# Performance work log

Measured on AMD Instinct MI355X. Metric: run time of the kernel, lower is better.

The kernel has to match this reference:

```python
import jax, jax.numpy as jnp
import numpy as np

ATTN_LEN = 128  # init_kwargs attn_len


def _lstm(x, Wih, Whh, bih, bhh):
    """PyTorch-style LSTM (gate order i,f,g,o), scanning over axis 0 of x.
    x: (S, N, H_in) -> (S, N, H). Matches nn.LSTM applied to the given layout."""
    H = Whh.shape[1]
    n = x.shape[1]
    xp = x @ Wih.T + bih + bhh  # precompute input projection, fold both biases

    def step(carry, xt):
        h, c = carry
        gates = xt + h @ Whh.T
        i, f, g, o = jnp.split(gates, 4, axis=-1)
        i = jax.nn.sigmoid(i)
        f = jax.nn.sigmoid(f)
        g = jnp.tanh(g)
        o = jax.nn.sigmoid(o)
        c = f * c + i * g
        h = o * jnp.tanh(c)
        return (h, c), h

    init = (jnp.zeros((n, H), x.dtype), jnp.zeros((n, H), x.dtype))
    _, hs = jax.lax.scan(step, init, xp)
    return hs


def setup_inputs() -> dict:
    key = jax.random.key(0)
    ks = jax.random.split(key, 16)
    F_in, H = 257, 256
    B, T = 8, 2048
    s = 1.0 / np.sqrt(H)

    def w(k, shape):
        return jax.random.uniform(k, shape, jnp.float32, -s, s)

    return {
        "x": jax.random.normal(ks[0], (B, T, F_in), jnp.float32),
        "feat_w": w(ks[1], (H, F_in)), "feat_b": w(ks[2], (H,)),
        "k_Wih": w(ks[3], (4 * H, H)), "k_Whh": w(ks[4], (4 * H, H)),
        "k_bih": w(ks[5], (4 * H,)), "k_bhh": w(ks[6], (4 * H,)),
        "q_Wih": w(ks[7], (4 * H, H)), "q_Whh": w(ks[8], (4 * H, H)),
        "q_bih": w(ks[9], (4 * H,)), "q_bhh": w(ks[10], (4 * H,)),
        "score_w": w(ks[11], (H, H)),
        "enhance_w": w(ks[12], (H, 2 * H)), "enhance_b": w(ks[13], (H,)),
        "mask_w": w(ks[14], (F_in, H)), "mask_b": w(ks[15], (F_in,)),
    }


def reference(x, feat_w, feat_b, k_Wih, k_Whh, k_bih, k_bhh,
              q_Wih, q_Whh, q_bih, q_bhh, score_w,
              enhance_w, enhance_b, mask_w, mask_b):
    input_x = x
    h = jnp.tanh(x @ feat_w.T + feat_b)          # (B,T,H); dropout_p=0 -> identity
    # Faithful to source: nn.LSTM without batch_first scans along dim0 of x.
    k = _lstm(h, k_Wih, k_Whh, k_bih, k_bhh)     # (B,T,H)
    q = _lstm(h, q_Wih, q_Whh, q_bih, q_bhh)     # stacked_encoder=False -> q_enc(x)

    # bmm(score(q), k^T): batched over dim0, attention over dims 1-2
    s = jnp.einsum('bth,bsh->bts', q @ score_w.T, k)
    e = jnp.exp(s - jnp.max(s, axis=-1, keepdims=True))
    T = s.shape[-1]
    band = jnp.tril(jnp.ones((T, T), x.dtype)) * jnp.triu(jnp.ones((T, T), x.dtype), -ATTN_LEN)
    w_ = e * band                                 # tril then triu(-attn_len)
    w_ = w_ / (jnp.sum(w_, axis=-1, keepdims=True) + 1e-10)
    c = jnp.einsum('bts,bsh->bth', w_, k)

    out = jnp.tanh(jnp.concatenate([c, q], axis=-1) @ enhance_w.T + enhance_b)
    m = jax.nn.sigmoid(out @ mask_w.T + mask_b)
    return input_x * m, w_
```

## Files before the change

kernel.cpp:

```cpp
#include <hip/hip_runtime.h>
#include <math.h>


#define Bq 8
#define Tq 2048
#define Fq 257
#define Hq 256
#define Gq 1024
#define TH (Tq*Hq)
#define KW 192
#define PLD 40
#define KTLD 40
#define Mq (Bq*Tq)

typedef __bf16 bf16_t;
typedef __bf16 bf16x8 __attribute__((ext_vector_type(8)));
typedef float f32x4 __attribute__((ext_vector_type(4)));

__device__ __forceinline__ float sigf(float x) { return 1.0f / (1.0f + __expf(-x)); }
__device__ __forceinline__ float tanh_f(float x) { return 1.0f - 2.0f / (__expf(2.0f * x) + 1.0f); }

#define CV_X   (Mq*288)
#define CV_FW  (256*288)
#define CV_WIH (2048*256)
#define CV_WHH (2048*256)
#define CV_SC  (256*256)
#define CV_EN  (256*512)
#define CV_MK  (384*256)
#define CV_O1  CV_X
#define CV_O2  (CV_O1+CV_FW)
#define CV_O3  (CV_O2+CV_WIH)
#define CV_O4  (CV_O3+CV_WHH)
#define CV_O5  (CV_O4+CV_SC)
#define CV_O6  (CV_O5+CV_EN)
#define CV_TOT (CV_O6+CV_MK)

__global__ __launch_bounds__(256) void cvt_all(
    const float* __restrict__ x, const float* __restrict__ feat_w,
    const float* __restrict__ kWih, const float* __restrict__ kWhh,
    const float* __restrict__ qWih, const float* __restrict__ qWhh,
    const float* __restrict__ scorew, const float* __restrict__ enhw,
    const float* __restrict__ maskw, bf16_t* __restrict__ dst)
{
    const int base = (blockIdx.x * 256 + threadIdx.x) * 8;
    if (base >= CV_TOT) return;
    bf16_t v[8];
#pragma unroll
    for (int e = 0; e < 8; ++e) {
        const int i = base + e;
        float f;
        if (i < CV_O1)      { const int r = i / 288, c = i - r * 288;
                              f = (c < Fq) ? x[(size_t)r * Fq + c] : 0.0f; }
        else if (i < CV_O2) { const int i2 = i - CV_O1, r = i2 / 288, c = i2 - r * 288;
                              f = (c < Fq) ? feat_w[r * Fq + c] : 0.0f; }
        else if (i < CV_O3) { const int i2 = i - CV_O2, r = i2 >> 8, c = i2 & 255;
                              f = (r < 1024) ? kWih[r * 256 + c] : qWih[(r - 1024) * 256 + c]; }
        else if (i < CV_O4) { const int i2 = i - CV_O3, r = i2 >> 8, c = i2 & 255;
                              f = (r < 1024) ? kWhh[r * 256 + c] : qWhh[(r - 1024) * 256 + c]; }
        else if (i < CV_O5) { f = scorew[i - CV_O4]; }
        else if (i < CV_O6) { f = enhw[i - CV_O5]; }
        else                { const int i2 = i - CV_O6, r = i2 >> 8, c = i2 & 255;
                              f = (r < Fq) ? maskw[r * 256 + c] : 0.0f; }
        v[e] = (bf16_t)f;
    }
    *(bf16x8*)(dst + base) = *(bf16x8*)v;
}

__global__ void bias_fold(const float* __restrict__ kbih, const float* __restrict__ kbhh,
                          const float* __restrict__ qbih, const float* __restrict__ qbhh,
                          float* __restrict__ out)
{
    const int i = blockIdx.x * 256 + threadIdx.x;
    out[i] = (i < 1024) ? kbih[i] + kbhh[i] : qbih[i - 1024] + qbhh[i - 1024];
}

__device__ __forceinline__ const bf16_t* seg_ptr(
    const bf16_t* __restrict__ A1, int lda1, int K1,
    const bf16_t* __restrict__ A2, int lda2, int row, int k, int col8)
{
    return (k < K1) ? A1 + (size_t)row * lda1 + k + col8
                    : A2 + (size_t)row * lda2 + (k - K1) + col8;
}

template<int ACT, bool MULX, bool BF16OUT, bool F32OUT>
__global__ __launch_bounds__(256) void gemm_mfma(
    const bf16_t* __restrict__ A1, int lda1, int K1,
    const bf16_t* __restrict__ A2, int lda2, int K2,
    const bf16_t* __restrict__ W,
    const float* __restrict__ bias,
    const float* __restrict__ xm, int ldx,
    float* __restrict__ out, bf16_t* __restrict__ outbf, int ldo, int Nlog)
{
    __shared__ __align__(16) bf16_t As[64 * 32];
    __shared__ __align__(16) bf16_t Ws[128 * 32];
    const int tid = threadIdx.x;
    const int lane = tid & 63;
    const int wave = tid >> 6;
    const int wr = wave >> 1, wc = wave & 1;
    const int fr = lane & 15;
    const int fo = (lane >> 4) * 8;
    const int srow = tid >> 2;
    const int scol = (tid & 3) * 8;
    const int m0 = blockIdx.y * 64, n0 = blockIdx.x * 128;

    const int K = K1 + K2;
    const int ldw = K;

    uint4 ar = *(const uint4*)seg_ptr(A1, lda1, K1, A2, lda2, m0 + srow, 0, scol);
    uint4 w0 = *(const uint4*)(W + (size_t)(n0 + srow)      * ldw + scol);
    uint4 w1 = *(const uint4*)(W + (size_t)(n0 + srow + 64) * ldw + scol);

    f32x4 acc[2][4] = {};
    for (int k0 = 0; k0 < K; k0 += 32) {
        __syncthreads();
        *(uint4*)&As[srow * 32 + scol]        = ar;
        *(uint4*)&Ws[srow * 32 + scol]        = w0;
        *(uint4*)&Ws[(srow + 64) * 32 + scol] = w1;
        if (k0 + 32 < K) {
            ar = *(const uint4*)seg_ptr(A1, lda1, K1, A2, lda2, m0 + srow, k0 + 32, scol);
            w0 = *(const uint4*)(W + (size_t)(n0 + srow)      * ldw + k0 + 32 + scol);
            w1 = *(const uint4*)(W + (size_t)(n0 + srow + 64) * ldw + k0 + 32 + scol);
        }
        __syncthreads();
        bf16x8 af[2], bfr[4];
#pragma unroll
        for (int i = 0; i < 2; ++i) af[i]  = *(const bf16x8*)&As[(wr * 32 + i * 16 + fr) * 32 + fo];
#pragma unroll
        for (int j = 0; j < 4; ++j) bfr[j] = *(const bf16x8*)&Ws[(wc * 64 + j * 16 + fr) * 32 + fo];
#pragma unroll
        for (int i = 0; i < 2; ++i)
#pragma unroll
            for (int j = 0; j < 4; ++j)
                acc[i][j] = __builtin_amdgcn_mfma_f32_16x16x32_bf16(af[i], bfr[j], acc[i][j], 0, 0, 0);
    }

    const int rbase = (lane >> 4) * 4;
#pragma unroll
    for (int i = 0; i < 2; ++i) {
#pragma unroll
        for (int j = 0; j < 4; ++j) {
            const int n = n0 + wc * 64 + j * 16 + fr;
            if (n >= Nlog) continue;
            const float bv = bias ? bias[n] : 0.0f;
            const int m = m0 + wr * 32 + i * 16 + rbase;
#pragma unroll
            for (int r = 0; r < 4; ++r) {
                float v = acc[i][j][r] + bv;
                if (ACT == 1) v = tanh_f(v);
                else if (ACT == 2) v = sigf(v);
                if (MULX) v *= xm[(size_t)(m + r) * ldx + n];
                if (F32OUT) out[(size_t)(m + r) * ldo + n] = v;
                if (BF16OUT) outbf[(size_t)(m + r) * ldo + n] = (bf16_t)v;
            }
        }
    }
}

__global__ __launch_bounds__(256) void lstm_step(
    const bf16_t* __restrict__ hkp, const bf16_t* __restrict__ hqp,
    const bf16_t* __restrict__ Whh_all,
    const float* __restrict__ xp_b,
    float* __restrict__ ck, float* __restrict__ cq,
    bf16_t* __restrict__ hk, bf16_t* __restrict__ hq)
{
    __shared__ __align__(16) bf16_t As[64 * 32];
    __shared__ __align__(16) bf16_t Ws[128 * 32];
    const int z = blockIdx.z;
    const bf16_t* hprev = z ? hqp : hkp;
    const bf16_t* Wbase = Whh_all + (size_t)z * 1024 * 256;
    float* c     = z ? cq : ck;
    bf16_t* hout = z ? hq : hk;

    const int tid = threadIdx.x, lane = tid & 63, wave = tid >> 6;
    const int wr = wave >> 1, wc = wave & 1;
    const int fr = lane & 15, rg = lane >> 4, fo = rg * 8;
    const int m0 = blockIdx.y * 64;
    const int jb = blockIdx.x * 32;

    f32x4 acc[2][4] = {};

    if (hprev) {
        const int arow = tid >> 2, acol = (tid & 3) * 8;
        const int s0 = tid >> 2, s1 = s0 + 64;
        const int wn0 = ((s0 >> 5) * 256) + jb + (s0 & 31);
        const int wn1 = ((s1 >> 5) * 256) + jb + (s1 & 31);
        uint4 ar  = *(const uint4*)(hprev + (size_t)(m0 + arow) * Hq + acol);
        uint4 w0r = *(const uint4*)(Wbase + (size_t)wn0 * 256 + acol);
        uint4 w1r = *(const uint4*)(Wbase + (size_t)wn1 * 256 + acol);
#pragma unroll
        for (int t = 0; t < 8; ++t) {
            if (t) __syncthreads();
            *(uint4*)&As[arow * 32 + acol] = ar;
            *(uint4*)&Ws[s0 * 32 + acol]   = w0r;
            *(uint4*)&Ws[s1 * 32 + acol]   = w1r;
            if (t < 7) {
                const int k = (t + 1) * 32;
                ar  = *(const uint4*)(hprev + (size_t)(m0 + arow) * Hq + k + acol);
                w0r = *(const uint4*)(Wbase + (size_t)wn0 * 256 + k + acol);
                w1r = *(const uint4*)(Wbase + (size_t)wn1 * 256 + k + acol);
            }
            __syncthreads();
            bf16x8 af[2], bg[4];
#pragma unroll
            for (int i = 0; i < 2; ++i) af[i] = *(const bf16x8*)&As[(wr * 32 + i * 16 + fr) * 32 + fo];
#pragma unroll
            for (int g = 0; g < 4; ++g) bg[g] = *(const bf16x8*)&Ws[(g * 32 + wc * 16 + fr) * 32 + fo];
#pragma unroll
            for (int i = 0; i < 2; ++i)
#pragma unroll
                for (int g = 0; g < 4; ++g)
                    acc[i][g] = __builtin_amdgcn_mfma_f32_16x16x32_bf16(af[i], bg[g], acc[i][g], 0, 0, 0);
        }
    }

    const int j = jb + wc * 16 + fr;
#pragma unroll
    for (int i = 0; i < 2; ++i) {
#pragma unroll
        for (int r = 0; r < 4; ++r) {
            const int t = m0 + wr * 32 + i * 16 + rg * 4 + r;
            const float* xpr = xp_b + (size_t)t * 2048 + (size_t)z * 1024;
            const float gi = acc[i][0][r] + xpr[j];
            const float gf = acc[i][1][r] + xpr[256 + j];
            const float gg = acc[i][2][r] + xpr[512 + j];
            const float go = acc[i][3][r] + xpr[768 + j];
            const size_t ix = (size_t)t * Hq + j;
            const float cn = sigf(gf) * c[ix] + sigf(gi) * tanh_f(gg);
            c[ix] = cn;
            hout[ix] = (bf16_t)(sigf(go) * tanh_f(cn));
        }
    }
}

__global__ __launch_bounds__(256) void band_fused(
    const bf16_t* __restrict__ qsbf, const bf16_t* __restrict__ kbf,
    float* __restrict__ out1, bf16_t* __restrict__ c_att)
{
    __shared__ __align__(16) bf16_t Ks[8 * KW * 32];
    __shared__ __align__(16) bf16_t P[6 * 64 * PLD];
    __shared__ __align__(16) bf16_t KT[256 * KTLD];

    const int b = blockIdx.y;
    const int t0 = blockIdx.x * 64;
    const int u0 = t0 - 128;
    const int tid = threadIdx.x, lane = tid & 63, w = tid >> 6;
    const int fr = lane & 15, rg = lane >> 4, fo = rg * 8;
    const size_t kbase = (size_t)b * Tq;

#pragma unroll
    for (int it = 0; it < 24; ++it) {
        const int idx = it * 256 + tid;
        const int n  = idx >> 5;
        const int c8 = (idx & 31) * 8;
        uint4 v = {0, 0, 0, 0};
        const int u = u0 + n;
        if (u >= 0) v = *(const uint4*)(kbf + (kbase + u) * (size_t)Hq + c8);
        *(uint4*)&Ks[((c8 >> 5) * KW + n) * 32 + (c8 & 31)] = v;
    }
    __syncthreads();

    f32x4 acc[12] = {};
    const bf16_t* qrow = qsbf + (kbase + t0 + 16 * w + fr) * (size_t)Hq;
#pragma unroll
    for (int ks = 0; ks < 8; ++ks) {
        const bf16x8 aq = *(const bf16x8*)(qrow + ks * 32 + fo);
#pragma unroll
        for (int jf = 0; jf < 12; ++jf) {
            const bf16x8 bk = *(const bf16x8*)&Ks[(ks * KW + jf * 16 + fr) * 32 + fo];
            acc[jf] = __builtin_amdgcn_mfma_f32_16x16x32_bf16(aq, bk, acc[jf], 0, 0, 0);
        }
    }

    const int jmin = (128 - t0) > 0 ? (128 - t0) : 0;
    float mx[4] = {-3e38f, -3e38f, -3e38f, -3e38f};
#pragma unroll
    for (int jf = 0; jf < 12; ++jf)
#pragma unroll
        for (int r = 0; r < 4; ++r) {
            const int i = 16 * w + rg * 4 + r;
            const int j = jf * 16 + fr;
            if (j >= i && j <= i + 128 && j >= jmin)
                mx[r] = fmaxf(mx[r], acc[jf][r]);
        }
#pragma unroll
    for (int d = 1; d < 16; d <<= 1)
#pragma unroll
        for (int r = 0; r < 4; ++r) mx[r] = fmaxf(mx[r], __shfl_xor(mx[r], d));

    float ex[12][4];
    float sm[4] = {0.0f, 0.0f, 0.0f, 0.0f};
#pragma unroll
    for (int jf = 0; jf < 12; ++jf)
#pragma unroll
        for (int r = 0; r < 4; ++r) {
            const int i = 16 * w + rg * 4 + r;
            const int j = jf * 16 + fr;
            const bool v = (j >= i && j <= i + 128 && j >= jmin);
            const float e = v ? __expf(acc[jf][r] - mx[r]) : 0.0f;
            ex[jf][r] = e;
            sm[r] += e;
        }
#pragma unroll
    for (int d = 1; d < 16; d <<= 1)
#pragma unroll
        for (int r = 0; r < 4; ++r) sm[r] += __shfl_xor(sm[r], d);
    float inv[4];
#pragma unroll
    for (int r = 0; r < 4; ++r) inv[r] = 1.0f / (sm[r] + 1e-10f);

#pragma unroll
    for (int jf = 0; jf < 12; ++jf)
#pragma unroll
        for (int r = 0; r < 4; ++r) {
            const int i = 16 * w + rg * 4 + r;
            const int j = jf * 16 + fr;
            const float wv = ex[jf][r] * inv[r];
            if (u0 + j >= 0)
                out1[(kbase + t0 + i) * (size_t)Tq + (u0 + j)] = wv;
            P[((j >> 5) * 64 + i) * PLD + (j & 31)] = (bf16_t)wv;
        }

    {
        const int c4l = (u0 > 0 ? u0 : 0) >> 2;
        const int c4r = (u0 + KW) >> 2;
        const float4 z4 = {0.0f, 0.0f, 0.0f, 0.0f};
        for (int rr = 0; rr < 16; ++rr) {
            float* rowp = out1 + (kbase + t0 + 16 * w + rr) * (size_t)Tq;
            for (int c4 = lane; c4 < c4l; c4 += 64)
                *(float4*)(rowp + 4 * c4) = z4;
            for (int c4 = c4r + lane; c4 < Tq / 4; c4 += 64)
                *(float4*)(rowp + 4 * c4) = z4;
        }
    }

    f32x4 cacc[16] = {};
    for (int jc = 0; jc < 6; ++jc) {
        __syncthreads();
#pragma unroll
        for (int it = 0; it < 4; ++it) {
            const int idx = it * 256 + tid;
            const int jl = idx >> 5;
            const int hc = (idx & 31) * 8;
            const bf16x8 kv = *(const bf16x8*)&Ks[((hc >> 5) * KW + jc * 32 + jl) * 32 + (hc & 31)];
#pragma unroll
            for (int e = 0; e < 8; ++e) KT[(hc + e) * KTLD + jl] = kv[e];
        }
        __syncthreads();
        const bf16x8 pa = *(const bf16x8*)&P[(jc * 64 + 16 * w + fr) * PLD + fo];
#pragma unroll
        for (int hf = 0; hf < 16; ++hf) {
            const bf16x8 bk = *(const bf16x8*)&KT[(hf * 16 + fr) * KTLD + fo];
            cacc[hf] = __builtin_amdgcn_mfma_f32_16x16x32_bf16(pa, bk, cacc[hf], 0, 0, 0);
        }
    }

#pragma unroll
    for (int hf = 0; hf < 16; ++hf)
#pragma unroll
        for (int r = 0; r < 4; ++r) {
            const int i = 16 * w + rg * 4 + r;
            c_att[(kbase + t0 + i) * (size_t)Hq + hf * 16 + fr] = (bf16_t)cacc[hf][r];
        }
}

extern "C" void kernel_launch(void* const* d_in, const int* in_sizes, int n_in,
                              void* d_out, int out_size, void* d_ws, size_t ws_size,
                              hipStream_t stream)
{
    (void)in_sizes; (void)n_in; (void)out_size; (void)ws_size;
    const float* x        = (const float*)d_in[0];
    const float* feat_w   = (const float*)d_in[1];
    const float* feat_b   = (const float*)d_in[2];
    const float* k_Wih    = (const float*)d_in[3];
    const float* k_Whh    = (const float*)d_in[4];
    const float* k_bih    = (const float*)d_in[5];
    const float* k_bhh    = (const float*)d_in[6];
    const float* q_Wih    = (const float*)d_in[7];
    const float* q_Whh    = (const float*)d_in[8];
    const float* q_bih    = (const float*)d_in[9];
    const float* q_bhh    = (const float*)d_in[10];
    const float* score_w  = (const float*)d_in[11];
    const float* enhance_w= (const float*)d_in[12];
    const float* enhance_b= (const float*)d_in[13];
    const float* mask_w   = (const float*)d_in[14];
    const float* mask_b   = (const float*)d_in[15];

    float* out0 = (float*)d_out;
    float* out1 = out0 + (size_t)Bq * Tq * Fq;

    float* cst      = (float*)d_ws;
    float* bias_all = cst + (size_t)2 * TH;
    float* xp       = bias_all + 2048;
    bf16_t* cvd = (bf16_t*)(xp + (size_t)Mq * 2048);
    bf16_t* xbf     = cvd;
    bf16_t* featw   = cvd + CV_O1;
    bf16_t* Wih_all = cvd + CV_O2;
    bf16_t* Whh_all = cvd + CV_O3;
    bf16_t* scw     = cvd + CV_O4;
    bf16_t* enw     = cvd + CV_O5;
    bf16_t* mkw     = cvd + CV_O6;
    bf16_t* hfeatbf = cvd + CV_TOT;
    bf16_t* hkbf    = hfeatbf + (size_t)Mq * Hq;
    bf16_t* hqbf    = hkbf + (size_t)Bq * TH;
    bf16_t* cattb   = hqbf + (size_t)Bq * TH;

    float* ck = cst;
    float* cq = cst + TH;

    hipMemsetAsync(cst, 0, (size_t)2 * TH * sizeof(float), stream);

    cvt_all<<<CV_TOT / 8 / 256, 256, 0, stream>>>(
        x, feat_w, k_Wih, k_Whh, q_Wih, q_Whh, score_w, enhance_w, mask_w, cvd);
    bias_fold<<<8, 256, 0, stream>>>(k_bih, k_bhh, q_bih, q_bhh, bias_all);

    gemm_mfma<1, false, true, false><<<dim3(2, Mq / 64), 256, 0, stream>>>(
        xbf, 288, 288, nullptr, 0, 0, featw, feat_b, nullptr, 0,
        nullptr, hfeatbf, Hq, 1 << 30);

    gemm_mfma<0, false, false, true><<<dim3(16, Mq / 64), 256, 0, stream>>>(
        hfeatbf, Hq, Hq, nullptr, 0, 0, Wih_all, bias_all, nullptr, 0,
        xp, nullptr, 2048, 2048);

    for (int b = 0; b < Bq; ++b) {
        const bf16_t* pk = b ? hkbf + (size_t)(b - 1) * TH : nullptr;
        const bf16_t* pq = b ? hqbf + (size_t)(b - 1) * TH : nullptr;
        lstm_step<<<dim3(8, Tq / 64, 2), 256, 0, stream>>>(
            pk, pq, Whh_all, xp + (size_t)b * Tq * 2048, ck, cq,
            hkbf + (size_t)b * TH, hqbf + (size_t)b * TH);
    }

    bf16_t* qsbf = xbf;
    gemm_mfma<0, false, true, false><<<dim3(2, Mq / 64), 256, 0, stream>>>(
        hqbf, Hq, Hq, nullptr, 0, 0, scw, nullptr, nullptr, 0,
        nullptr, qsbf, Hq, 1 << 30);

    band_fused<<<dim3(Tq / 64, Bq), 256, 0, stream>>>(qsbf, hkbf, out1, cattb);

    bf16_t* outh = hfeatbf;
    gemm_mfma<1, false, true, false><<<dim3(2, Mq / 64), 256, 0, stream>>>(
        cattb, Hq, Hq, hqbf, Hq, Hq, enw, enhance_b, nullptr, 0,
        nullptr, outh, Hq, 1 << 30);

    gemm_mfma<2, true, false, true><<<dim3(3, Mq / 64), 256, 0, stream>>>(
        outh, Hq, Hq, nullptr, 0, 0, mkw, mask_b, x, Fq,
        out0, nullptr, Fq, Fq);
}
```

Measured before the change: 254.1 us.

## Fuse LSTM input projection into recurrent step kernel with concatenated weights

Drops the separate input-projection GEMM and its large fp32 xp buffer. Each LSTM step kernel now runs a K=512 GEMM over [h_feat, h_prev] against concatenated [Wih|Whh] bf16 weights and adds the folded bias in the epilogue. The first step is a template specialization that skips the previous-hidden part and the c read, which removes the memset. Bias folding also moves into the conversion kernel, so two launches go away. The recurrent chain does more GEMM work per step, but the step kernels no longer write and re-read the 128MB fp32 intermediate.

```diff
diff --git a/kernel.cpp b/kernel.cpp
--- a/kernel.cpp
+++ b/kernel.cpp
@@ -6,7 +6,6 @@
 #define Tq 2048
 #define Fq 257
 #define Hq 256
-#define Gq 1024
 #define TH (Tq*Hq)
 #define KW 192
 #define PLD 40
@@ -22,28 +21,41 @@
 
 #define CV_X   (Mq*288)
 #define CV_FW  (256*288)
-#define CV_WIH (2048*256)
-#define CV_WHH (2048*256)
+#define CV_WK  (1024*512)
+#define CV_WQ  (1024*512)
 #define CV_SC  (256*256)
 #define CV_EN  (256*512)
 #define CV_MK  (384*256)
 #define CV_O1  CV_X
 #define CV_O2  (CV_O1+CV_FW)
-#define CV_O3  (CV_O2+CV_WIH)
-#define CV_O4  (CV_O3+CV_WHH)
+#define CV_O3  (CV_O2+CV_WK)
+#define CV_O4  (CV_O3+CV_WQ)
 #define CV_O5  (CV_O4+CV_SC)
 #define CV_O6  (CV_O5+CV_EN)
 #define CV_TOT (CV_O6+CV_MK)
+#define CVB    (CV_TOT/8/256)
 
 __global__ __launch_bounds__(256) void cvt_all(
     const float* __restrict__ x, const float* __restrict__ feat_w,
     const float* __restrict__ kWih, const float* __restrict__ kWhh,
     const float* __restrict__ qWih, const float* __restrict__ qWhh,
     const float* __restrict__ scorew, const float* __restrict__ enhw,
-    const float* __restrict__ maskw, bf16_t* __restrict__ dst)
-{
+    const float* __restrict__ maskw, bf16_t* __restrict__ dst,
+    const float* __restrict__ kbih, const float* __restrict__ kbhh,
+    const float* __restrict__ qbih, const float* __restrict__ qbhh,
+    float* __restrict__ bias_all)
+{
+    if (blockIdx.x == CVB) {
+        const int i0 = threadIdx.x * 8;
+#pragma unroll
+        for (int e = 0; e < 8; ++e) {
+            const int i = i0 + e;
+            bias_all[i] = (i < 1024) ? kbih[i] + kbhh[i]
+                                     : qbih[i - 1024] + qbhh[i - 1024];
+        }
+        return;
+    }
     const int base = (blockIdx.x * 256 + threadIdx.x) * 8;
-    if (base >= CV_TOT) return;
     bf16_t v[8];
 #pragma unroll
     for (int e = 0; e < 8; ++e) {
@@ -53,10 +65,10 @@
                               f = (c < Fq) ? x[(size_t)r * Fq + c] : 0.0f; }
         else if (i < CV_O2) { const int i2 = i - CV_O1, r = i2 / 288, c = i2 - r * 288;
                               f = (c < Fq) ? feat_w[r * Fq + c] : 0.0f; }
-        else if (i < CV_O3) { const int i2 = i - CV_O2, r = i2 >> 8, c = i2 & 255;
-                              f = (r < 1024) ? kWih[r * 256 + c] : qWih[(r - 1024) * 256 + c]; }
-        else if (i < CV_O4) { const int i2 = i - CV_O3, r = i2 >> 8, c = i2 & 255;
-                              f = (r < 1024) ? kWhh[r * 256 + c] : qWhh[(r - 1024) * 256 + c]; }
+        else if (i < CV_O3) { const int i2 = i - CV_O2, r = i2 >> 9, c = i2 & 511;
+                              f = (c < 256) ? kWih[r * 256 + c] : kWhh[r * 256 + c - 256]; }
+        else if (i < CV_O4) { const int i2 = i - CV_O3, r = i2 >> 9, c = i2 & 511;
+                              f = (c < 256) ? qWih[r * 256 + c] : qWhh[r * 256 + c - 256]; }
         else if (i < CV_O5) { f = scorew[i - CV_O4]; }
         else if (i < CV_O6) { f = enhw[i - CV_O5]; }
         else                { const int i2 = i - CV_O6, r = i2 >> 8, c = i2 & 255;
@@ -64,14 +76,6 @@
         v[e] = (bf16_t)f;
     }
     *(bf16x8*)(dst + base) = *(bf16x8*)v;
-}
-
-__global__ void bias_fold(const float* __restrict__ kbih, const float* __restrict__ kbhh,
-                          const float* __restrict__ qbih, const float* __restrict__ qbhh,
-                          float* __restrict__ out)
-{
-    const int i = blockIdx.x * 256 + threadIdx.x;
-    out[i] = (i < 1024) ? kbih[i] + kbhh[i] : qbih[i - 1024] + qbhh[i - 1024];
 }
 
 __device__ __forceinline__ const bf16_t* seg_ptr(
@@ -156,19 +160,20 @@
     }
 }
 
+template<bool FIRST>
 __global__ __launch_bounds__(256) void lstm_step(
+    const bf16_t* __restrict__ hfb,
     const bf16_t* __restrict__ hkp, const bf16_t* __restrict__ hqp,
-    const bf16_t* __restrict__ Whh_all,
-    const float* __restrict__ xp_b,
-    float* __restrict__ ck, float* __restrict__ cq,
+    const bf16_t* __restrict__ Wall, const float* __restrict__ bias_all,
+    float* __restrict__ cst,
     bf16_t* __restrict__ hk, bf16_t* __restrict__ hq)
 {
     __shared__ __align__(16) bf16_t As[64 * 32];
     __shared__ __align__(16) bf16_t Ws[128 * 32];
     const int z = blockIdx.z;
     const bf16_t* hprev = z ? hqp : hkp;
-    const bf16_t* Wbase = Whh_all + (size_t)z * 1024 * 256;
-    float* c     = z ? cq : ck;
+    const bf16_t* Wz = Wall + (size_t)z * (1024 * 512);
+    float* c     = cst + (size_t)z * TH;
     bf16_t* hout = z ? hq : hk;
 
     const int tid = threadIdx.x, lane = tid & 63, wave = tid >> 6;
@@ -177,59 +182,64 @@
     const int m0 = blockIdx.y * 64;
     const int jb = blockIdx.x * 32;
 
+    const int s0 = tid >> 2, acol = (tid & 3) * 8;
+    const int s1 = s0 + 64;
+    const int wn0 = ((s0 >> 5) * 256) + jb + (s0 & 31);
+    const int wn1 = ((s1 >> 5) * 256) + jb + (s1 & 31);
+
+    constexpr int NIT = FIRST ? 8 : 16;
+
     f32x4 acc[2][4] = {};
 
-    if (hprev) {
-        const int arow = tid >> 2, acol = (tid & 3) * 8;
-        const int s0 = tid >> 2, s1 = s0 + 64;
-        const int wn0 = ((s0 >> 5) * 256) + jb + (s0 & 31);
-        const int wn1 = ((s1 >> 5) * 256) + jb + (s1 & 31);
-        uint4 ar  = *(const uint4*)(hprev + (size_t)(m0 + arow) * Hq + acol);
-        uint4 w0r = *(const uint4*)(Wbase + (size_t)wn0 * 256 + acol);
-        uint4 w1r = *(const uint4*)(Wbase + (size_t)wn1 * 256 + acol);
-#pragma unroll
-        for (int t = 0; t < 8; ++t) {
-            if (t) __syncthreads();
-            *(uint4*)&As[arow * 32 + acol] = ar;
-            *(uint4*)&Ws[s0 * 32 + acol]   = w0r;
-            *(uint4*)&Ws[s1 * 32 + acol]   = w1r;
-            if (t < 7) {
-                const int k = (t + 1) * 32;
-                ar  = *(const uint4*)(hprev + (size_t)(m0 + arow) * Hq + k + acol);
-                w0r = *(const uint4*)(Wbase + (size_t)wn0 * 256 + k + acol);
-                w1r = *(const uint4*)(Wbase + (size_t)wn1 * 256 + k + acol);
-            }
-            __syncthreads();
-            bf16x8 af[2], bg[4];
-#pragma unroll
-            for (int i = 0; i < 2; ++i) af[i] = *(const bf16x8*)&As[(wr * 32 + i * 16 + fr) * 32 + fo];
-#pragma unroll
-            for (int g = 0; g < 4; ++g) bg[g] = *(const bf16x8*)&Ws[(g * 32 + wc * 16 + fr) * 32 + fo];
-#pragma unroll
-            for (int i = 0; i < 2; ++i)
-#pragma unroll
-                for (int g = 0; g < 4; ++g)
-                    acc[i][g] = __builtin_amdgcn_mfma_f32_16x16x32_bf16(af[i], bg[g], acc[i][g], 0, 0, 0);
-        }
+    uint4 ar  = *(const uint4*)(hfb + (size_t)(m0 + s0) * Hq + acol);
+    uint4 w0r = *(const uint4*)(Wz + (size_t)wn0 * 512 + acol);
+    uint4 w1r = *(const uint4*)(Wz + (size_t)wn1 * 512 + acol);
+#pragma unroll
+    for (int t = 0; t < NIT; ++t) {
+        if (t) __syncthreads();
+        *(uint4*)&As[s0 * 32 + acol] = ar;
+        *(uint4*)&Ws[s0 * 32 + acol] = w0r;
+        *(uint4*)&Ws[s1 * 32 + acol] = w1r;
+        if (t + 1 < NIT) {
+            const int tn = t + 1;
+            ar  = (tn < 8)
+                ? *(const uint4*)(hfb   + (size_t)(m0 + s0) * Hq + tn * 32 + acol)
+                : *(const uint4*)(hprev + (size_t)(m0 + s0) * Hq + (tn - 8) * 32 + acol);
+            w0r = *(const uint4*)(Wz + (size_t)wn0 * 512 + tn * 32 + acol);
+            w1r = *(const uint4*)(Wz + (size_t)wn1 * 512 + tn * 32 + acol);
+        }
+        __syncthreads();
+        bf16x8 af[2], bg[4];
+#pragma unroll
+        for (int i = 0; i < 2; ++i) af[i] = *(const bf16x8*)&As[(wr * 32 + i * 16 + fr) * 32 + fo];
+#pragma unroll
+        for (int g = 0; g < 4; ++g) bg[g] = *(const bf16x8*)&Ws[(g * 32 + wc * 16 + fr) * 32 + fo];
+#pragma unroll
+        for (int i = 0; i < 2; ++i)
+#pragma unroll
+            for (int g = 0; g < 4; ++g)
+                acc[i][g] = __builtin_amdgcn_mfma_f32_16x16x32_bf16(af[i], bg[g], acc[i][g], 0, 0, 0);
     }
 
     const int j = jb + wc * 16 + fr;
-#pragma unroll
-    for (int i = 0; i < 2; ++i) {
+    float bs[4];
+#pragma unroll
+    for (int g = 0; g < 4; ++g) bs[g] = bias_all[z * 1024 + g * 256 + j];
+#pragma unroll
+    for (int i = 0; i < 2; ++i)
 #pragma unroll
         for (int r = 0; r < 4; ++r) {
             const int t = m0 + wr * 32 + i * 16 + rg * 4 + r;
-            const float* xpr = xp_b + (size_t)t * 2048 + (size_t)z * 1024;
-            const float gi = acc[i][0][r] + xpr[j];
-            const float gf = acc[i][1][r] + xpr[256 + j];
-            const float gg = acc[i][2][r] + xpr[512 + j];
-            const float go = acc[i][3][r] + xpr[768 + j];
             const size_t ix = (size_t)t * Hq + j;
-            const float cn = sigf(gf) * c[ix] + sigf(gi) * tanh_f(gg);
+            const float gi = acc[i][0][r] + bs[0];
+            const float gf = acc[i][1][r] + bs[1];
+            const float gg = acc[i][2][r] + bs[2];
+            const float go = acc[i][3][r] + bs[3];
+            const float cn = FIRST ? sigf(gi) * tanh_f(gg)
+                                   : sigf(gf) * c[ix] + sigf(gi) * tanh_f(gg);
             c[ix] = cn;
             hout[ix] = (bf16_t)(sigf(go) * tanh_f(cn));
         }
-    }
 }
 
 __global__ __launch_bounds__(256) void band_fused(
@@ -390,12 +400,10 @@
 
     float* cst      = (float*)d_ws;
     float* bias_all = cst + (size_t)2 * TH;
-    float* xp       = bias_all + 2048;
-    bf16_t* cvd = (bf16_t*)(xp + (size_t)Mq * 2048);
+    bf16_t* cvd = (bf16_t*)(bias_all + 2048);
     bf16_t* xbf     = cvd;
     bf16_t* featw   = cvd + CV_O1;
-    bf16_t* Wih_all = cvd + CV_O2;
-    bf16_t* Whh_all = cvd + CV_O3;
+    bf16_t* Wall    = cvd + CV_O2;
     bf16_t* scw     = cvd + CV_O4;
     bf16_t* enw     = cvd + CV_O5;
     bf16_t* mkw     = cvd + CV_O6;
@@ -404,30 +412,22 @@
     bf16_t* hqbf    = hkbf + (size_t)Bq * TH;
     bf16_t* cattb   = hqbf + (size_t)Bq * TH;
 
-    float* ck = cst;
-    float* cq = cst + TH;
-
-    hipMemsetAsync(cst, 0, (size_t)2 * TH * sizeof(float), stream);
-
-    cvt_all<<<CV_TOT / 8 / 256, 256, 0, stream>>>(
-        x, feat_w, k_Wih, k_Whh, q_Wih, q_Whh, score_w, enhance_w, mask_w, cvd);
-    bias_fold<<<8, 256, 0, stream>>>(k_bih, k_bhh, q_bih, q_bhh, bias_all);
+    cvt_all<<<CVB + 1, 256, 0, stream>>>(
+        x, feat_w, k_Wih, k_Whh, q_Wih, q_Whh, score_w, enhance_w, mask_w, cvd,
+        k_bih, k_bhh, q_bih, q_bhh, bias_all);
 
     gemm_mfma<1, false, true, false><<<dim3(2, Mq / 64), 256, 0, stream>>>(
         xbf, 288, 288, nullptr, 0, 0, featw, feat_b, nullptr, 0,
         nullptr, hfeatbf, Hq, 1 << 30);
 
-    gemm_mfma<0, false, false, true><<<dim3(16, Mq / 64), 256, 0, stream>>>(
-        hfeatbf, Hq, Hq, nullptr, 0, 0, Wih_all, bias_all, nullptr, 0,
-        xp, nullptr, 2048, 2048);
-
-    for (int b = 0; b < Bq; ++b) {
-        const bf16_t* pk = b ? hkbf + (size_t)(b - 1) * TH : nullptr;
-        const bf16_t* pq = b ? hqbf + (size_t)(b - 1) * TH : nullptr;
-        lstm_step<<<dim3(8, Tq / 64, 2), 256, 0, stream>>>(
-            pk, pq, Whh_all, xp + (size_t)b * Tq * 2048, ck, cq,
+    lstm_step<true><<<dim3(8, Tq / 64, 2), 256, 0, stream>>>(
+        hfeatbf, nullptr, nullptr, Wall, bias_all, cst, hkbf, hqbf);
+    for (int b = 1; b < Bq; ++b)
+        lstm_step<false><<<dim3(8, Tq / 64, 2), 256, 0, stream>>>(
+            hfeatbf + (size_t)b * TH,
+            hkbf + (size_t)(b - 1) * TH, hqbf + (size_t)(b - 1) * TH,
+            Wall, bias_all, cst,
             hkbf + (size_t)b * TH, hqbf + (size_t)b * TH);
-    }
 
     bf16_t* qsbf = xbf;
     gemm_mfma<0, false, true, false><<<dim3(2, Mq / 64), 256, 0, stream>>>(
```

Measured after the change: 209.9 us. 17.4% less time.

## Fuse first LSTM step into input-projection GEMM and merge bias fold into conversion

Applied to the files above, without the earlier changes.

Replaces the generic input-projection GEMM with a gate-interleaved xp_gemm kernel. For the first batch slice (zero initial state) it applies the LSTM cell directly and writes c and h, so there is no xp write for that slice, no memset of the cell state, and no first lstm_step launch. The bias folding moves into an extra block of the conversion kernel, which saves one launch. The costs are a specialised kernel layout and dropping the forget-gate term, which relies on the initial state being zero.

```diff
diff --git a/kernel.cpp b/kernel.cpp
--- a/kernel.cpp
+++ b/kernel.cpp
@@ -6,7 +6,6 @@
 #define Tq 2048
 #define Fq 257
 #define Hq 256
-#define Gq 1024
 #define TH (Tq*Hq)
 #define KW 192
 #define PLD 40
@@ -34,16 +33,29 @@
 #define CV_O5  (CV_O4+CV_SC)
 #define CV_O6  (CV_O5+CV_EN)
 #define CV_TOT (CV_O6+CV_MK)
+#define CVB    (CV_TOT/8/256)
 
 __global__ __launch_bounds__(256) void cvt_all(
     const float* __restrict__ x, const float* __restrict__ feat_w,
     const float* __restrict__ kWih, const float* __restrict__ kWhh,
     const float* __restrict__ qWih, const float* __restrict__ qWhh,
     const float* __restrict__ scorew, const float* __restrict__ enhw,
-    const float* __restrict__ maskw, bf16_t* __restrict__ dst)
-{
+    const float* __restrict__ maskw, bf16_t* __restrict__ dst,
+    const float* __restrict__ kbih, const float* __restrict__ kbhh,
+    const float* __restrict__ qbih, const float* __restrict__ qbhh,
+    float* __restrict__ bias_all)
+{
+    if (blockIdx.x == CVB) {
+        const int i0 = threadIdx.x * 8;
+#pragma unroll
+        for (int e = 0; e < 8; ++e) {
+            const int i = i0 + e;
+            bias_all[i] = (i < 1024) ? kbih[i] + kbhh[i]
+                                     : qbih[i - 1024] + qbhh[i - 1024];
+        }
+        return;
+    }
     const int base = (blockIdx.x * 256 + threadIdx.x) * 8;
-    if (base >= CV_TOT) return;
     bf16_t v[8];
 #pragma unroll
     for (int e = 0; e < 8; ++e) {
@@ -66,14 +78,6 @@
     *(bf16x8*)(dst + base) = *(bf16x8*)v;
 }
 
-__global__ void bias_fold(const float* __restrict__ kbih, const float* __restrict__ kbhh,
-                          const float* __restrict__ qbih, const float* __restrict__ qbhh,
-                          float* __restrict__ out)
-{
-    const int i = blockIdx.x * 256 + threadIdx.x;
-    out[i] = (i < 1024) ? kbih[i] + kbhh[i] : qbih[i - 1024] + qbhh[i - 1024];
-}
-
 __device__ __forceinline__ const bf16_t* seg_ptr(
     const bf16_t* __restrict__ A1, int lda1, int K1,
     const bf16_t* __restrict__ A2, int lda2, int row, int k, int col8)
@@ -156,6 +160,95 @@
     }
 }
 
+__global__ __launch_bounds__(256) void xp_gemm(
+    const bf16_t* __restrict__ hfeat,
+    const bf16_t* __restrict__ Wih_all,
+    const float* __restrict__ bias_all,
+    float* __restrict__ xp,
+    float* __restrict__ cst,
+    bf16_t* __restrict__ hk0, bf16_t* __restrict__ hq0)
+{
+    __shared__ __align__(16) bf16_t As[64 * 32];
+    __shared__ __align__(16) bf16_t Ws[128 * 32];
+    const int z = blockIdx.z;
+    const bf16_t* Wz = Wih_all + (size_t)z * (1024 * 256);
+
+    const int tid = threadIdx.x, lane = tid & 63, wave = tid >> 6;
+    const int wr = wave >> 1, wc = wave & 1;
+    const int fr = lane & 15, rg = lane >> 4, fo = rg * 8;
+    const int m0 = blockIdx.y * 64;
+    const int jb = blockIdx.x * 32;
+
+    const int s0 = tid >> 2, acol = (tid & 3) * 8;
+    const int s1 = s0 + 64;
+    const int wn0 = ((s0 >> 5) * 256) + jb + (s0 & 31);
+    const int wn1 = ((s1 >> 5) * 256) + jb + (s1 & 31);
+
+    f32x4 acc[2][4] = {};
+    uint4 ar  = *(const uint4*)(hfeat + (size_t)(m0 + s0) * Hq + acol);
+    uint4 w0r = *(const uint4*)(Wz + (size_t)wn0 * 256 + acol);
+    uint4 w1r = *(const uint4*)(Wz + (size_t)wn1 * 256 + acol);
+#pragma unroll
+    for (int t = 0; t < 8; ++t) {
+        if (t) __syncthreads();
+        *(uint4*)&As[s0 * 32 + acol] = ar;
+        *(uint4*)&Ws[s0 * 32 + acol] = w0r;
+        *(uint4*)&Ws[s1 * 32 + acol] = w1r;
+        if (t < 7) {
+            const int k = (t + 1) * 32;
+            ar  = *(const uint4*)(hfeat + (size_t)(m0 + s0) * Hq + k + acol);
+            w0r = *(const uint4*)(Wz + (size_t)wn0 * 256 + k + acol);
+            w1r = *(const uint4*)(Wz + (size_t)wn1 * 256 + k + acol);
+        }
+        __syncthreads();
+        bf16x8 af[2], bg[4];
+#pragma unroll
+        for (int i = 0; i < 2; ++i) af[i] = *(const bf16x8*)&As[(wr * 32 + i * 16 + fr) * 32 + fo];
+#pragma unroll
+        for (int g = 0; g < 4; ++g) bg[g] = *(const bf16x8*)&Ws[(g * 32 + wc * 16 + fr) * 32 + fo];
+#pragma unroll
+        for (int i = 0; i < 2; ++i)
+#pragma unroll
+            for (int g = 0; g < 4; ++g)
+                acc[i][g] = __builtin_amdgcn_mfma_f32_16x16x32_bf16(af[i], bg[g], acc[i][g], 0, 0, 0);
+    }
+
+    const int j = jb + wc * 16 + fr;
+    float bs[4];
+#pragma unroll
+    for (int g = 0; g < 4; ++g) bs[g] = bias_all[z * 1024 + g * 256 + j];
+
+    if (m0 < Tq) {
+        float* c = cst + (size_t)z * TH;
+        bf16_t* hout = z ? hq0 : hk0;
+#pragma unroll
+        for (int i = 0; i < 2; ++i)
+#pragma unroll
+            for (int r = 0; r < 4; ++r) {
+                const int t = m0 + wr * 32 + i * 16 + rg * 4 + r;
+                const size_t ix = (size_t)t * Hq + j;
+                const float gi = acc[i][0][r] + bs[0];
+                const float gg = acc[i][2][r] + bs[2];
+                const float go = acc[i][3][r] + bs[3];
+                const float cn = sigf(gi) * tanh_f(gg);
+                c[ix] = cn;
+                hout[ix] = (bf16_t)(sigf(go) * tanh_f(cn));
+            }
+    } else {
+#pragma unroll
+        for (int i = 0; i < 2; ++i)
+#pragma unroll
+            for (int r = 0; r < 4; ++r) {
+                const int t = m0 + wr * 32 + i * 16 + rg * 4 + r;
+                float* xpr = xp + (size_t)t * 2048 + (size_t)z * 1024;
+                xpr[j]       = acc[i][0][r] + bs[0];
+                xpr[256 + j] = acc[i][1][r] + bs[1];
+                xpr[512 + j] = acc[i][2][r] + bs[2];
+                xpr[768 + j] = acc[i][3][r] + bs[3];
+            }
+    }
+}
+
 __global__ __launch_bounds__(256) void lstm_step(
     const bf16_t* __restrict__ hkp, const bf16_t* __restrict__ hqp,
     const bf16_t* __restrict__ Whh_all,
@@ -179,7 +272,7 @@
 
     f32x4 acc[2][4] = {};
 
-    if (hprev) {
+    {
         const int arow = tid >> 2, acol = (tid & 3) * 8;
         const int s0 = tid >> 2, s1 = s0 + 64;
         const int wn0 = ((s0 >> 5) * 256) + jb + (s0 & 31);
@@ -407,27 +500,22 @@
     float* ck = cst;
     float* cq = cst + TH;
 
-    hipMemsetAsync(cst, 0, (size_t)2 * TH * sizeof(float), stream);
-
-    cvt_all<<<CV_TOT / 8 / 256, 256, 0, stream>>>(
-        x, feat_w, k_Wih, k_Whh, q_Wih, q_Whh, score_w, enhance_w, mask_w, cvd);
-    bias_fold<<<8, 256, 0, stream>>>(k_bih, k_bhh, q_bih, q_bhh, bias_all);
+    cvt_all<<<CVB + 1, 256, 0, stream>>>(
+        x, feat_w, k_Wih, k_Whh, q_Wih, q_Whh, score_w, enhance_w, mask_w, cvd,
+        k_bih, k_bhh, q_bih, q_bhh, bias_all);
 
     gemm_mfma<1, false, true, false><<<dim3(2, Mq / 64), 256, 0, stream>>>(
         xbf, 288, 288, nullptr, 0, 0, featw, feat_b, nullptr, 0,
         nullptr, hfeatbf, Hq, 1 << 30);
 
-    gemm_mfma<0, false, false, true><<<dim3(16, Mq / 64), 256, 0, stream>>>(
-        hfeatbf, Hq, Hq, nullptr, 0, 0, Wih_all, bias_all, nullptr, 0,
-        xp, nullptr, 2048, 2048);
-
-    for (int b = 0; b < Bq; ++b) {
-        const bf16_t* pk = b ? hkbf + (size_t)(b - 1) * TH : nullptr;
-        const bf16_t* pq = b ? hqbf + (size_t)(b - 1) * TH : nullptr;
+    xp_gemm<<<dim3(8, Mq / 64, 2), 256, 0, stream>>>(
+        hfeatbf, Wih_all, bias_all, xp, cst, hkbf, hqbf);
+
+    for (int b = 1; b < Bq; ++b)
         lstm_step<<<dim3(8, Tq / 64, 2), 256, 0, stream>>>(
-            pk, pq, Whh_all, xp + (size_t)b * Tq * 2048, ck, cq,
+            hkbf + (size_t)(b - 1) * TH, hqbf + (size_t)(b - 1) * TH,
+            Whh_all, xp + (size_t)b * Tq * 2048, ck, cq,
             hkbf + (size_t)b * TH, hqbf + (size_t)b * TH);
-    }
 
     bf16_t* qsbf = xbf;
     gemm_mfma<0, false, true, false><<<dim3(2, Mq / 64), 256, 0, stream>>>(
```

Result: faster. 244.5 us (-3.8%).
